# Kernel tuning notes

Measured on AMD Instinct MI355X. Metric: run time of the kernel, lower is better.

Reference implementation:

```python
import jax, jax.numpy as jnp
import numpy as np

K = 1024   # codebook size
C = 8      # codebook channels
D = K // C # per-channel code dim = 128
BETA = 0.25
B = 8192   # batch of latent vectors, each of size C*D = K


def setup_inputs() -> dict:
    key = jax.random.key(0)
    k1, k2, k3 = jax.random.split(key, 3)
    latents = jax.random.normal(k1, (B, C * D), dtype=jnp.float32)
    # nn.Embedding(K, D) init: uniform(-1/K, 1/K)
    embedding = jax.random.uniform(k2, (K, D), dtype=jnp.float32,
                                   minval=-1.0 / K, maxval=1.0 / K)
    k = jax.random.randint(k3, (C,), 0, 8, dtype=jnp.int32)
    return {"latents": latents, "embedding": embedding, "k": k}


def reference(latents, embedding, k):
    sg = jax.lax.stop_gradient
    flat = latents.reshape(-1, D)                                  # [B*C, D]
    # squared euclidean distance to every code: [B*C, K]
    dist = (jnp.sum(flat ** 2, axis=1, keepdims=True)
            + jnp.sum(embedding ** 2, axis=1)
            - 2.0 * (flat @ embedding.T))
    order = jnp.argsort(dist, axis=1).reshape(-1, C, K)            # [B, C, K]
    # per channel c, pick the k[c]-th nearest code index
    sel = jnp.take_along_axis(order, k[None, :, None], axis=2)[..., 0]  # [B, C]
    # one-hot @ embedding == plain gather of selected rows
    quantized = embedding[sel.reshape(-1)].reshape(latents.shape)  # [B, C*D]
    commitment_loss = jnp.mean((sg(quantized) - latents) ** 2)
    embedding_loss = jnp.mean((quantized - sg(latents)) ** 2)
    vq_loss = BETA * commitment_loss + embedding_loss
    # straight-through estimator
    quantized_st = latents + sg(quantized - latents)
    return quantized_st, vq_loss
```

## Files before the change

kernel.cpp:

```cpp
#include <hip/hip_runtime.h>

#define KDIM   128
#define NELEM  8388608

typedef __attribute__((ext_vector_type(4))) float f32x4;
typedef __attribute__((ext_vector_type(2))) int   int2v;

__device__ inline f32x4 mfma8(long long a, long long b, f32x4 c) {
  return __builtin_amdgcn_mfma_f32_16x16x32_fp8_fp8(a, b, c, 0, 0, 0);
}
__device__ inline void gload16(const void* g, void* l) {
  __builtin_amdgcn_global_load_lds(
      (const __attribute__((address_space(1))) unsigned*)g,
      (__attribute__((address_space(3))) unsigned*)l, 16, 0, 0);
}
__device__ inline long long pk8(float4 v0, float4 v1) {
  int lo = __builtin_amdgcn_cvt_pk_fp8_f32(v0.x, v0.y, 0, false);
  lo     = __builtin_amdgcn_cvt_pk_fp8_f32(v0.z, v0.w, lo, true);
  int hi = __builtin_amdgcn_cvt_pk_fp8_f32(v1.x, v1.y, 0, false);
  hi     = __builtin_amdgcn_cvt_pk_fp8_f32(v1.z, v1.w, hi, true);
  int2v t; t.x = lo; t.y = hi;
  return __builtin_bit_cast(long long, t);
}
__device__ inline float packk(float s, int c) {
  return __builtin_bit_cast(float,
      (__builtin_bit_cast(unsigned, s) & 0xFFFFFC00u) | (unsigned)c);
}
__device__ inline float sumsq(float4 a, float4 b) {
  return a.x*a.x + a.y*a.y + a.z*a.z + a.w*a.w + b.x*b.x + b.y*b.y + b.z*b.z + b.w*b.w;
}
__device__ inline void merge8(float (&t)[8], int msk) {
  float o[8];
#pragma unroll
  for (int p = 0; p < 8; ++p) o[p] = __shfl_xor(t[p], msk);
  float m[8];
#pragma unroll
  for (int p = 0; p < 8; ++p) m[p] = fmaxf(t[p], o[7 - p]);
#pragma unroll
  for (int s = 4; s; s >>= 1)
#pragma unroll
    for (int i = 0; i < 8; ++i)
      if (!(i & s)) {
        float x = fmaxf(m[i], m[i | s]);
        m[i | s] = fminf(m[i], m[i | s]);
        m[i] = x;
      }
#pragma unroll
  for (int p = 0; p < 8; ++p) t[p] = m[p];
}
__device__ inline void ins8(float (&top)[8], float x) {
#pragma unroll
  for (int p = 0; p < 8; ++p) {
    float mx = fmaxf(top[p], x);
    x = fminf(top[p], x);
    top[p] = mx;
  }
}

__global__ void vq_prep(const float* __restrict__ emb, unsigned char* __restrict__ ebf8,
                        float* __restrict__ esqm, unsigned long long* __restrict__ lossAcc,
                        unsigned* __restrict__ cnt) {
  int j = blockIdx.x, d = threadIdx.x;
  float v = emb[j * KDIM + d];
  float vs = v * 1024.0f;
  int p = __builtin_amdgcn_cvt_pk_fp8_f32(vs, vs, 0, false);
  ebf8[j * KDIM + (d ^ ((j & 15) << 3))] = (unsigned char)(p & 0xFF);
  float s = v * v;
#pragma unroll
  for (int m = 1; m <= 32; m <<= 1) s += __shfl_xor(s, m);
  __shared__ float w[2];
  if ((d & 63) == 0) w[d >> 6] = s;
  __syncthreads();
  if (d == 0) esqm[j] = -512.0f * (w[0] + w[1]);
  if (j == 0 && d == 0) { lossAcc[0] = 0ULL; cnt[0] = 0u; }
}

__device__ inline void write_rows(const float* __restrict__ emb, float* __restrict__ outp,
                                  int grow0, int idx, int lane) {
#pragma unroll 4
  for (int r = 0; r < 16; ++r) {
    int s2 = __shfl(idx, r);
    float2 qv = *(const float2*)(emb + (size_t)s2 * KDIM + lane * 2);
    *(float2*)(outp + (size_t)(grow0 + r) * KDIM + lane * 2) = qv;
  }
}

__global__ __launch_bounds__(512, 1) void vq_main(
    const float* __restrict__ lat, const float* __restrict__ emb,
    const int* __restrict__ ksel, const unsigned char* __restrict__ ebf8,
    const float* __restrict__ esqm, float* __restrict__ out,
    unsigned long long* __restrict__ lossAcc, unsigned* __restrict__ cnt,
    float* __restrict__ loss) {
  __shared__ __align__(16) unsigned char smem[131072 + 4096 + 64];
  float* esqmLds = (float*)(smem + 131072);
  float* wLds    = (float*)(smem + 131072 + 4096);

  const int tid = threadIdx.x, lane = tid & 63, wid = tid >> 6;
  const int n = lane & 15, hi = lane >> 4;
  const int gR0 = blockIdx.x * 256;

  const float* rp0 = lat + (size_t)(gR0 + wid * 32 + n) * KDIM + hi * 8;
  const float* rp1 = rp0 + 16 * KDIM;
  float4 p0[4], p1[4], q0[4], q1[4];
#pragma unroll
  for (int ks = 0; ks < 4; ++ks) {
    p0[ks] = *(const float4*)(rp0 + ks * 32);
    p1[ks] = *(const float4*)(rp0 + ks * 32 + 4);
    q0[ks] = *(const float4*)(rp1 + ks * 32);
    q1[ks] = *(const float4*)(rp1 + ks * 32 + 4);
  }
  {
    const char* src = (const char*)ebf8 + tid * 16;
    char* dst = (char*)smem + tid * 16;
#pragma unroll
    for (int qq = 0; qq < 16; ++qq) gload16(src + qq * 8192, dst + qq * 8192);
    if (tid < 256) gload16((const char*)esqm + tid * 16, (char*)esqmLds + tid * 16);
  }
  float fsq0, fsq1;
  long long b00, b01, b02, b03, b10, b11, b12, b13;
  {
    float s0 = 0.f, s1 = 0.f;
#pragma unroll
    for (int ks = 0; ks < 4; ++ks) {
      s0 += sumsq(p0[ks], p1[ks]);
      s1 += sumsq(q0[ks], q1[ks]);
    }
    s0 += __shfl_xor(s0, 16); s0 += __shfl_xor(s0, 32);
    s1 += __shfl_xor(s1, 16); s1 += __shfl_xor(s1, 32);
    fsq0 = s0; fsq1 = s1;
    b00 = pk8(p0[0], p1[0]); b01 = pk8(p0[1], p1[1]);
    b02 = pk8(p0[2], p1[2]); b03 = pk8(p0[3], p1[3]);
    b10 = pk8(q0[0], q1[0]); b11 = pk8(q0[1], q1[1]);
    b12 = pk8(q0[2], q1[2]); b13 = pk8(q0[3], q1[3]);
  }
  asm volatile("s_waitcnt vmcnt(0)" ::: "memory");
  __builtin_amdgcn_s_barrier();

  const unsigned char* ab = smem + n * 128 + ((hi ^ (n & 3)) << 3);
  const int nh = n >> 2;
  const unsigned char* bk0 = ab + ((0 ^ nh) << 5);
  const unsigned char* bk1 = ab + ((1 ^ nh) << 5);
  const unsigned char* bk2 = ab + ((2 ^ nh) << 5);
  const unsigned char* bk3 = ab + ((3 ^ nh) << 5);

  const float NINF = __builtin_bit_cast(float, 0xFF800000u);
  float top0[8], top1[8];
#pragma unroll
  for (int p = 0; p < 8; ++p) { top0[p] = NINF; top1[p] = NINF; }

  const int stw = wid * 4;
#pragma unroll 4
  for (int pp = 0; pp < 32; ++pp) {
    const int g = (pp + stw) & 31;
    const int off = g * 4096;
    const float* eb = esqmLds + g * 32 + hi * 4;
    f32x4 e0 = *(const f32x4*)(eb);
    f32x4 e1 = *(const f32x4*)(eb + 16);
    long long t0 = *(const long long*)(bk0 + off);
    long long t1 = *(const long long*)(bk1 + off);
    long long t2 = *(const long long*)(bk2 + off);
    long long t3 = *(const long long*)(bk3 + off);
    long long u0 = *(const long long*)(bk0 + off + 2048);
    long long u1 = *(const long long*)(bk1 + off + 2048);
    long long u2 = *(const long long*)(bk2 + off + 2048);
    long long u3 = *(const long long*)(bk3 + off + 2048);
    f32x4 a0 = e0, a1 = e1, a2 = e0, a3 = e1;
    a0 = mfma8(t0, b00, a0); a1 = mfma8(u0, b00, a1);
    a2 = mfma8(t0, b10, a2); a3 = mfma8(u0, b10, a3);
    a0 = mfma8(t1, b01, a0); a1 = mfma8(u1, b01, a1);
    a2 = mfma8(t1, b11, a2); a3 = mfma8(u1, b11, a3);
    a0 = mfma8(t2, b02, a0); a1 = mfma8(u2, b02, a1);
    a2 = mfma8(t2, b12, a2); a3 = mfma8(u2, b12, a3);
    a0 = mfma8(t3, b03, a0); a1 = mfma8(u3, b03, a1);
    a2 = mfma8(t3, b13, a2); a3 = mfma8(u3, b13, a3);

    const int cb = g * 32 + hi * 4;
    {
      float k0 = packk(a0[0], cb + 0),  k1 = packk(a0[1], cb + 1);
      float k2 = packk(a0[2], cb + 2),  k3 = packk(a0[3], cb + 3);
      float k4 = packk(a1[0], cb + 16), k5 = packk(a1[1], cb + 17);
      float k6 = packk(a1[2], cb + 18), k7 = packk(a1[3], cb + 19);
      float x = fmaxf(fmaxf(fmaxf(k0, k1), fmaxf(k2, k3)),
                      fmaxf(fmaxf(k4, k5), fmaxf(k6, k7)));
      ins8(top0, x);
    }
    {
      float k0 = packk(a2[0], cb + 0),  k1 = packk(a2[1], cb + 1);
      float k2 = packk(a2[2], cb + 2),  k3 = packk(a2[3], cb + 3);
      float k4 = packk(a3[0], cb + 16), k5 = packk(a3[1], cb + 17);
      float k6 = packk(a3[2], cb + 18), k7 = packk(a3[3], cb + 19);
      float x = fmaxf(fmaxf(fmaxf(k0, k1), fmaxf(k2, k3)),
                      fmaxf(fmaxf(k4, k5), fmaxf(k6, k7)));
      ins8(top1, x);
    }
  }

  int kk = ksel[lane & 7];
  kk = kk < 0 ? 0 : (kk > 7 ? 7 : kk);

  merge8(top0, 16); merge8(top0, 32);
  float sel0 = top0[0];
#pragma unroll
  for (int p = 1; p < 8; ++p) sel0 = (kk == p) ? top0[p] : sel0;
  unsigned sb0 = __builtin_bit_cast(unsigned, sel0);
  int idx0 = (int)(sb0 & 1023u);
  float rl0 = fsq0 - __builtin_bit_cast(float, sb0 & 0xFFFFFC00u) * (1.0f / 512.0f);
  write_rows(emb, out, gR0 + wid * 32, idx0, lane);

  merge8(top1, 16); merge8(top1, 32);
  float sel1 = top1[0];
#pragma unroll
  for (int p = 1; p < 8; ++p) sel1 = (kk == p) ? top1[p] : sel1;
  unsigned sb1 = __builtin_bit_cast(unsigned, sel1);
  int idx1 = (int)(sb1 & 1023u);
  float rl1 = fsq1 - __builtin_bit_cast(float, sb1 & 0xFFFFFC00u) * (1.0f / 512.0f);
  write_rows(emb, out, gR0 + wid * 32 + 16, idx1, lane);

  float c = (lane < 16) ? (rl0 + rl1) : 0.f;
#pragma unroll
  for (int m = 1; m <= 32; m <<= 1) c += __shfl_xor(c, m);
  if (lane == 0) wLds[wid] = c;
  __syncthreads();
  if (tid == 0) {
    double bs = 0.0;
#pragma unroll
    for (int w = 0; w < 8; ++w) bs += (double)wLds[w];
    long long iv = (long long)(bs * 1048576.0 + 0.5);
    atomicAdd(lossAcc, (unsigned long long)iv);
    __threadfence();
    unsigned done = atomicAdd(cnt, 1u);
    if (done == 255u) {
      unsigned long long tot = atomicAdd(lossAcc, 0ULL);
      loss[0] = (float)((double)(long long)tot * (1.25 / (1048576.0 * 8388608.0)));
    }
  }
}

extern "C" void kernel_launch(void* const* d_in, const int* in_sizes, int n_in,
                              void* d_out, int out_size, void* d_ws, size_t ws_size,
                              hipStream_t stream) {
  const float* lat = (const float*)d_in[0];
  const float* emb = (const float*)d_in[1];
  const int* ksel = (const int*)d_in[2];
  float* out = (float*)d_out;

  unsigned char* ebf8 = (unsigned char*)d_ws;
  float* esqm = (float*)((char*)d_ws + 131072);
  unsigned long long* lossAcc =
      (unsigned long long*)((char*)d_ws + 135168);
  unsigned* cnt = (unsigned*)((char*)d_ws + 135176);

  vq_prep<<<1024, 128, 0, stream>>>(emb, ebf8, esqm, lossAcc, cnt);
  vq_main<<<256, 512, 0, stream>>>(lat, emb, ksel, ebf8, esqm, out, lossAcc, cnt,
                                   out + NELEM);
}
```

Baseline: 44.85 us.

## Split codebook LDS load in halves to overlap second half with first-half scan

Codebook staging into LDS is split into two 64KB halves. The first half is scanned while the second half's async global-to-LDS loads are still in flight, with a wait and barrier only before the second half. The scan loop is fully unrolled per half and drops the per-wave rotated start. Packing is restructured so only the low within-group index is ORed into each element and the group offset is ORed once after the max. The aim is to hide codebook load latency behind MFMA work and trim per-element index arithmetic, at the cost of an extra barrier and possibly more LDS bank conflicts now that all waves start on the same group.

```diff
diff --git a/kernel.cpp b/kernel.cpp
--- a/kernel.cpp
+++ b/kernel.cpp
@@ -22,7 +22,7 @@
   int2v t; t.x = lo; t.y = hi;
   return __builtin_bit_cast(long long, t);
 }
-__device__ inline float packk(float s, int c) {
+__device__ inline float andor(float s, int c) {
   return __builtin_bit_cast(float,
       (__builtin_bit_cast(unsigned, s) & 0xFFFFFC00u) | (unsigned)c);
 }
@@ -54,6 +54,45 @@
     float mx = fmaxf(top[p], x);
     x = fminf(top[p], x);
     top[p] = mx;
+  }
+}
+
+struct Frags { long long b0[4], b1[4]; float fsq0, fsq1; };
+
+__device__ inline Frags make_frags(const float* __restrict__ lat, int row0, int row1,
+                                   int n, int hi) {
+  const float* rp0 = lat + (size_t)(row0 + n) * KDIM + hi * 8;
+  const float* rp1 = lat + (size_t)(row1 + n) * KDIM + hi * 8;
+  float4 p0[4], p1[4], q0[4], q1[4];
+#pragma unroll
+  for (int ks = 0; ks < 4; ++ks) {
+    p0[ks] = *(const float4*)(rp0 + ks * 32);
+    p1[ks] = *(const float4*)(rp0 + ks * 32 + 4);
+    q0[ks] = *(const float4*)(rp1 + ks * 32);
+    q1[ks] = *(const float4*)(rp1 + ks * 32 + 4);
+  }
+  Frags f;
+  float s0 = 0.f, s1 = 0.f;
+#pragma unroll
+  for (int ks = 0; ks < 4; ++ks) { s0 += sumsq(p0[ks], p1[ks]); s1 += sumsq(q0[ks], q1[ks]); }
+  s0 += __shfl_xor(s0, 16); s0 += __shfl_xor(s0, 32);
+  s1 += __shfl_xor(s1, 16); s1 += __shfl_xor(s1, 32);
+  f.fsq0 = s0; f.fsq1 = s1;
+#pragma unroll
+  for (int ks = 0; ks < 4; ++ks) {
+    f.b0[ks] = pk8(p0[ks], p1[ks]);
+    f.b1[ks] = pk8(q0[ks], q1[ks]);
+  }
+  return f;
+}
+
+__device__ inline void write_rows(const float* __restrict__ emb, float* __restrict__ outp,
+                                  int grow0, int idx, int lane) {
+#pragma unroll 4
+  for (int r = 0; r < 16; ++r) {
+    int s2 = __shfl(idx, r);
+    float2 qv = *(const float2*)(emb + (size_t)s2 * KDIM + lane * 2);
+    *(float2*)(outp + (size_t)(grow0 + r) * KDIM + lane * 2) = qv;
   }
 }
 
@@ -75,13 +114,66 @@
   if (j == 0 && d == 0) { lossAcc[0] = 0ULL; cnt[0] = 0u; }
 }
 
-__device__ inline void write_rows(const float* __restrict__ emb, float* __restrict__ outp,
-                                  int grow0, int idx, int lane) {
-#pragma unroll 4
-  for (int r = 0; r < 16; ++r) {
-    int s2 = __shfl(idx, r);
-    float2 qv = *(const float2*)(emb + (size_t)s2 * KDIM + lane * 2);
-    *(float2*)(outp + (size_t)(grow0 + r) * KDIM + lane * 2) = qv;
+template <int H>
+__device__ inline void scan_half(const unsigned char* smem, const float* esqmLds,
+                                 int n, int hi, const Frags& f, const int (&c8)[8],
+                                 float (&top0)[8], float (&top1)[8]) {
+  const unsigned char* ab = smem + H * 65536 + n * 128 + ((hi ^ (n & 3)) << 3);
+  const int nh = n >> 2;
+  const unsigned char* bk0 = ab + ((0 ^ nh) << 5);
+  const unsigned char* bk1 = ab + ((1 ^ nh) << 5);
+  const unsigned char* bk2 = ab + ((2 ^ nh) << 5);
+  const unsigned char* bk3 = ab + ((3 ^ nh) << 5);
+  const float* eb = esqmLds + H * 512 + hi * 4;
+#pragma unroll
+  for (int g = 0; g < 16; ++g) {
+    const int off = g * 4096;
+    f32x4 e0 = *(const f32x4*)(eb + g * 32);
+    f32x4 e1 = *(const f32x4*)(eb + g * 32 + 16);
+    long long t0 = *(const long long*)(bk0 + off);
+    long long t1 = *(const long long*)(bk1 + off);
+    long long t2 = *(const long long*)(bk2 + off);
+    long long t3 = *(const long long*)(bk3 + off);
+    long long u0 = *(const long long*)(bk0 + off + 2048);
+    long long u1 = *(const long long*)(bk1 + off + 2048);
+    long long u2 = *(const long long*)(bk2 + off + 2048);
+    long long u3 = *(const long long*)(bk3 + off + 2048);
+    f32x4 a0 = mfma8(t0, f.b0[0], e0);
+    f32x4 a1 = mfma8(u0, f.b0[0], e1);
+    f32x4 a2 = mfma8(t0, f.b1[0], e0);
+    f32x4 a3 = mfma8(u0, f.b1[0], e1);
+    a0 = mfma8(t1, f.b0[1], a0); a1 = mfma8(u1, f.b0[1], a1);
+    a2 = mfma8(t1, f.b1[1], a2); a3 = mfma8(u1, f.b1[1], a3);
+    a0 = mfma8(t2, f.b0[2], a0); a1 = mfma8(u2, f.b0[2], a1);
+    a2 = mfma8(t2, f.b1[2], a2); a3 = mfma8(u2, f.b1[2], a3);
+    a0 = mfma8(t3, f.b0[3], a0); a1 = mfma8(u3, f.b0[3], a1);
+    a2 = mfma8(t3, f.b1[3], a2); a3 = mfma8(u3, f.b1[3], a3);
+
+    const unsigned orv = (unsigned)(H * 512 + g * 32);
+    {
+      float k0 = andor(a0[0], c8[0]), k1 = andor(a0[1], c8[1]);
+      float k2 = andor(a0[2], c8[2]), k3 = andor(a0[3], c8[3]);
+      float k4 = andor(a1[0], c8[4]), k5 = andor(a1[1], c8[5]);
+      float k6 = andor(a1[2], c8[6]), k7 = andor(a1[3], c8[7]);
+      float m0 = fmaxf(fmaxf(k0, k1), k2);
+      float m1 = fmaxf(fmaxf(k3, k4), k5);
+      float m2 = fmaxf(fmaxf(k6, k7), m0);
+      float x = fmaxf(m1, m2);
+      x = __builtin_bit_cast(float, __builtin_bit_cast(unsigned, x) | orv);
+      ins8(top0, x);
+    }
+    {
+      float k0 = andor(a2[0], c8[0]), k1 = andor(a2[1], c8[1]);
+      float k2 = andor(a2[2], c8[2]), k3 = andor(a2[3], c8[3]);
+      float k4 = andor(a3[0], c8[4]), k5 = andor(a3[1], c8[5]);
+      float k6 = andor(a3[2], c8[6]), k7 = andor(a3[3], c8[7]);
+      float m0 = fmaxf(fmaxf(k0, k1), k2);
+      float m1 = fmaxf(fmaxf(k3, k4), k5);
+      float m2 = fmaxf(fmaxf(k6, k7), m0);
+      float x = fmaxf(m1, m2);
+      x = __builtin_bit_cast(float, __builtin_bit_cast(unsigned, x) | orv);
+      ins8(top1, x);
+    }
   }
 }
 
@@ -99,104 +191,41 @@
   const int n = lane & 15, hi = lane >> 4;
   const int gR0 = blockIdx.x * 256;
 
-  const float* rp0 = lat + (size_t)(gR0 + wid * 32 + n) * KDIM + hi * 8;
-  const float* rp1 = rp0 + 16 * KDIM;
-  float4 p0[4], p1[4], q0[4], q1[4];
-#pragma unroll
-  for (int ks = 0; ks < 4; ++ks) {
-    p0[ks] = *(const float4*)(rp0 + ks * 32);
-    p1[ks] = *(const float4*)(rp0 + ks * 32 + 4);
-    q0[ks] = *(const float4*)(rp1 + ks * 32);
-    q1[ks] = *(const float4*)(rp1 + ks * 32 + 4);
-  }
   {
     const char* src = (const char*)ebf8 + tid * 16;
     char* dst = (char*)smem + tid * 16;
 #pragma unroll
-    for (int qq = 0; qq < 16; ++qq) gload16(src + qq * 8192, dst + qq * 8192);
+    for (int q = 0; q < 8; ++q) gload16(src + q * 8192, dst + q * 8192);
     if (tid < 256) gload16((const char*)esqm + tid * 16, (char*)esqmLds + tid * 16);
   }
-  float fsq0, fsq1;
-  long long b00, b01, b02, b03, b10, b11, b12, b13;
-  {
-    float s0 = 0.f, s1 = 0.f;
-#pragma unroll
-    for (int ks = 0; ks < 4; ++ks) {
-      s0 += sumsq(p0[ks], p1[ks]);
-      s1 += sumsq(q0[ks], q1[ks]);
-    }
-    s0 += __shfl_xor(s0, 16); s0 += __shfl_xor(s0, 32);
-    s1 += __shfl_xor(s1, 16); s1 += __shfl_xor(s1, 32);
-    fsq0 = s0; fsq1 = s1;
-    b00 = pk8(p0[0], p1[0]); b01 = pk8(p0[1], p1[1]);
-    b02 = pk8(p0[2], p1[2]); b03 = pk8(p0[3], p1[3]);
-    b10 = pk8(q0[0], q1[0]); b11 = pk8(q0[1], q1[1]);
-    b12 = pk8(q0[2], q1[2]); b13 = pk8(q0[3], q1[3]);
-  }
+  Frags f = make_frags(lat, gR0 + wid * 32, gR0 + wid * 32 + 16, n, hi);
   asm volatile("s_waitcnt vmcnt(0)" ::: "memory");
   __builtin_amdgcn_s_barrier();
 
-  const unsigned char* ab = smem + n * 128 + ((hi ^ (n & 3)) << 3);
-  const int nh = n >> 2;
-  const unsigned char* bk0 = ab + ((0 ^ nh) << 5);
-  const unsigned char* bk1 = ab + ((1 ^ nh) << 5);
-  const unsigned char* bk2 = ab + ((2 ^ nh) << 5);
-  const unsigned char* bk3 = ab + ((3 ^ nh) << 5);
+  {
+    const char* src = (const char*)ebf8 + 65536 + tid * 16;
+    char* dst = (char*)smem + 65536 + tid * 16;
+#pragma unroll
+    for (int q = 0; q < 8; ++q) gload16(src + q * 8192, dst + q * 8192);
+  }
+
+  int c8[8];
+#pragma unroll
+  for (int r = 0; r < 4; ++r) { c8[r] = hi * 4 + r; c8[4 + r] = 16 + hi * 4 + r; }
 
   const float NINF = __builtin_bit_cast(float, 0xFF800000u);
   float top0[8], top1[8];
 #pragma unroll
   for (int p = 0; p < 8; ++p) { top0[p] = NINF; top1[p] = NINF; }
 
-  const int stw = wid * 4;
-#pragma unroll 4
-  for (int pp = 0; pp < 32; ++pp) {
-    const int g = (pp + stw) & 31;
-    const int off = g * 4096;
-    const float* eb = esqmLds + g * 32 + hi * 4;
-    f32x4 e0 = *(const f32x4*)(eb);
-    f32x4 e1 = *(const f32x4*)(eb + 16);
-    long long t0 = *(const long long*)(bk0 + off);
-    long long t1 = *(const long long*)(bk1 + off);
-    long long t2 = *(const long long*)(bk2 + off);
-    long long t3 = *(const long long*)(bk3 + off);
-    long long u0 = *(const long long*)(bk0 + off + 2048);
-    long long u1 = *(const long long*)(bk1 + off + 2048);
-    long long u2 = *(const long long*)(bk2 + off + 2048);
-    long long u3 = *(const long long*)(bk3 + off + 2048);
-    f32x4 a0 = e0, a1 = e1, a2 = e0, a3 = e1;
-    a0 = mfma8(t0, b00, a0); a1 = mfma8(u0, b00, a1);
-    a2 = mfma8(t0, b10, a2); a3 = mfma8(u0, b10, a3);
-    a0 = mfma8(t1, b01, a0); a1 = mfma8(u1, b01, a1);
-    a2 = mfma8(t1, b11, a2); a3 = mfma8(u1, b11, a3);
-    a0 = mfma8(t2, b02, a0); a1 = mfma8(u2, b02, a1);
-    a2 = mfma8(t2, b12, a2); a3 = mfma8(u2, b12, a3);
-    a0 = mfma8(t3, b03, a0); a1 = mfma8(u3, b03, a1);
-    a2 = mfma8(t3, b13, a2); a3 = mfma8(u3, b13, a3);
-
-    const int cb = g * 32 + hi * 4;
-    {
-      float k0 = packk(a0[0], cb + 0),  k1 = packk(a0[1], cb + 1);
-      float k2 = packk(a0[2], cb + 2),  k3 = packk(a0[3], cb + 3);
-      float k4 = packk(a1[0], cb + 16), k5 = packk(a1[1], cb + 17);
-      float k6 = packk(a1[2], cb + 18), k7 = packk(a1[3], cb + 19);
-      float x = fmaxf(fmaxf(fmaxf(k0, k1), fmaxf(k2, k3)),
-                      fmaxf(fmaxf(k4, k5), fmaxf(k6, k7)));
-      ins8(top0, x);
-    }
-    {
-      float k0 = packk(a2[0], cb + 0),  k1 = packk(a2[1], cb + 1);
-      float k2 = packk(a2[2], cb + 2),  k3 = packk(a2[3], cb + 3);
-      float k4 = packk(a3[0], cb + 16), k5 = packk(a3[1], cb + 17);
-      float k6 = packk(a3[2], cb + 18), k7 = packk(a3[3], cb + 19);
-      float x = fmaxf(fmaxf(fmaxf(k0, k1), fmaxf(k2, k3)),
-                      fmaxf(fmaxf(k4, k5), fmaxf(k6, k7)));
-      ins8(top1, x);
-    }
-  }
-
-  int kk = ksel[lane & 7];
-  kk = kk < 0 ? 0 : (kk > 7 ? 7 : kk);
+  scan_half<0>(smem, esqmLds, n, hi, f, c8, top0, top1);
+
+  asm volatile("s_waitcnt vmcnt(0)" ::: "memory");
+  __builtin_amdgcn_s_barrier();
+
+  scan_half<1>(smem, esqmLds, n, hi, f, c8, top0, top1);
+
+  int kk = ksel[lane & 7]; kk = kk < 0 ? 0 : (kk > 7 ? 7 : kk);
 
   merge8(top0, 16); merge8(top0, 32);
   float sel0 = top0[0];
@@ -204,7 +233,7 @@
   for (int p = 1; p < 8; ++p) sel0 = (kk == p) ? top0[p] : sel0;
   unsigned sb0 = __builtin_bit_cast(unsigned, sel0);
   int idx0 = (int)(sb0 & 1023u);
-  float rl0 = fsq0 - __builtin_bit_cast(float, sb0 & 0xFFFFFC00u) * (1.0f / 512.0f);
+  float rl0 = f.fsq0 - __builtin_bit_cast(float, sb0 & 0xFFFFFC00u) * (1.0f / 512.0f);
   write_rows(emb, out, gR0 + wid * 32, idx0, lane);
 
   merge8(top1, 16); merge8(top1, 32);
@@ -213,7 +242,7 @@
   for (int p = 1; p < 8; ++p) sel1 = (kk == p) ? top1[p] : sel1;
   unsigned sb1 = __builtin_bit_cast(unsigned, sel1);
   int idx1 = (int)(sb1 & 1023u);
-  float rl1 = fsq1 - __builtin_bit_cast(float, sb1 & 0xFFFFFC00u) * (1.0f / 512.0f);
+  float rl1 = f.fsq1 - __builtin_bit_cast(float, sb1 & 0xFFFFFC00u) * (1.0f / 512.0f);
   write_rows(emb, out, gR0 + wid * 32 + 16, idx1, lane);
 
   float c = (lane < 16) ? (rl0 + rl1) : 0.f;
```

After: 51.93 us. 1.16x slower.
